# Optimization experiments

Hardware: AMD Instinct MI355X
Metric: run time of the kernel (lower is better)

## Reference

```python
import jax, jax.numpy as jnp
import numpy as np

B, S, D_IN, D_H = 64, 512, 512, 1024

def setup_inputs() -> dict:
    key = jax.random.key(0)
    k1, k2 = jax.random.split(key)
    x = jax.random.normal(k1, (B, S, D_IN), dtype=jnp.float32)
    h0 = jnp.zeros((B, D_H), dtype=jnp.float32)
    # torch Linear(in+hid -> hid): weight [hid, in+hid]; we store transposed [in+hid, hid]
    W = jax.random.normal(k2, (D_IN + D_H, D_H), dtype=jnp.float32) * (1.0 / np.sqrt(D_IN + D_H))
    b = jnp.zeros((D_H,), dtype=jnp.float32)
    return {"x": x, "h0": h0, "W": W, "b": b}

def reference(x, h0, W, b):
    # h_t = tanh([x_t, h_{t-1}] @ W + b). Split W so the input projection
    # is one big batched GEMM outside the scan; recurrence handles Wh part.
    d_in = x.shape[-1]
    Wx, Wh = W[:d_in], W[d_in:]              # [D_in, H], [H, H]
    xproj = jnp.einsum('bsd,dh->bsh', x, Wx) + b  # [B, S, H]

    def step(h, xp_t):
        h_new = jnp.tanh(xp_t + h @ Wh)      # [B, H]
        return h_new, h_new

    # scan over time: move seq axis to front
    h_last, outs = jax.lax.scan(step, h0, jnp.swapaxes(xproj, 0, 1))
    return jnp.swapaxes(outs, 0, 1), h_last  # [B, S, H], [B, H]
```

## Files before the change

### kernel.cpp

```cpp
#include <hip/hip_runtime.h>
#include <hip/hip_bf16.h>
#include <stdint.h>

#define B_   64
#define S_   512
#define DIN  512
#define DH   1024
#define KTOT (DIN + DH)
#define NBG  4
#define NCG  32
#define BBLK 16
#define CBLK 32
#define NKC  (KTOT / 32)
#define NKX  (DIN / 32)

typedef __bf16 bf16x8 __attribute__((ext_vector_type(8)));
typedef float f32x4 __attribute__((ext_vector_type(4)));
typedef unsigned short ushort8v __attribute__((ext_vector_type(8)));
typedef unsigned short ushort4v __attribute__((ext_vector_type(4)));

static __device__ __forceinline__ unsigned short f2bf(float f) {
    union { __bf16 b; unsigned short u; } v; v.b = (__bf16)f; return v.u;
}
static __device__ __forceinline__ float fast_tanh(float x) {
    float e = __expf(2.0f * x);
    return 1.0f - 2.0f / (e + 1.0f);
}

__global__ void k_cvt_bf16(const float* __restrict__ src,
                           unsigned short* __restrict__ dst, int n4) {
    int i = blockIdx.x * blockDim.x + threadIdx.x;
    if (i < n4) {
        float4 v = ((const float4*)src)[i];
        ushort4v o;
        o.x = f2bf(v.x); o.y = f2bf(v.y); o.z = f2bf(v.z); o.w = f2bf(v.w);
        ((ushort4v*)dst)[i] = o;
    }
}

__global__ void k_swz_w(const float* __restrict__ W,
                        unsigned short* __restrict__ dst) {
    int u = blockIdx.x * blockDim.x + threadIdx.x;
    int lane = u & 63;
    int ntg  = (u >> 6) & 63;
    int kc   = u >> 12;
    int q = lane >> 4, n16 = lane & 15;
    int k0 = kc * 32 + q * 8;
    int n  = ntg * 16 + n16;
    ushort8v o;
#pragma unroll
    for (int i = 0; i < 8; ++i) o[i] = f2bf(W[(size_t)(k0 + i) * DH + n]);
    *(ushort8v*)(dst + (size_t)u * 8) = o;
}

#define SMEM_W_USH   (NKC * 2 * 64 * 8)
#define SMEM_P_PITCH 34
#define SMEM_P_FLT   (4 * 16 * SMEM_P_PITCH)
#define SMEM_BYTES   (SMEM_W_USH * 2 + SMEM_P_FLT * 4)

__global__ __launch_bounds__(256, 1) void k_rnn(
    const unsigned short* __restrict__ xb,
    const unsigned short* __restrict__ wswz,
    const float* __restrict__ h0,
    const float* __restrict__ bias,
    float* __restrict__ out,
    unsigned int* ring,
    int* flags)
{
    extern __shared__ char smem[];
    unsigned short* ldsW = (unsigned short*)smem;
    float* ldsP = (float*)(smem + SMEM_W_USH * 2);

    const int tid = threadIdx.x;
    const int bg = blockIdx.x >> 5;
    const int cg = blockIdx.x & 31;
    const int b0 = bg * BBLK;
    const int c0 = cg * CBLK;
    const int lane = tid & 63;
    const int wv = tid >> 6;
    const int q = lane >> 4;
    const int m16 = lane & 15;

    for (int c = tid; c < NKC * 2 * 64; c += 256) {
        int kc = c >> 7;
        int rem = c & 127;
        int l = rem >> 6;
        int ln = rem & 63;
        size_t src = ((size_t)(kc * 64 + 2 * cg + l) * 64 + ln) * 8;
        int dst = ((kc * 2 + l) * 64 + ln) * 8;
        *(ushort8v*)(ldsW + dst) = *(const ushort8v*)(wswz + src);
    }

    const int em = tid >> 4;
    const int np = (tid & 15) * 2;
    const float bias0 = bias[c0 + np];
    const float bias1 = bias[c0 + np + 1];

    __syncthreads();

    for (int t = 0; t < S_; ++t) {
        f32x4 acc0 = {0.f, 0.f, 0.f, 0.f}, acc1 = {0.f, 0.f, 0.f, 0.f};
        {
            bf16x8 ax[4];
            const unsigned short* xrow =
                xb + ((size_t)(b0 + m16) * S_ + t) * DIN + q * 8;
#pragma unroll
            for (int kk = 0; kk < 4; ++kk)
                ax[kk] = *(const bf16x8*)(xrow + (wv * 4 + kk) * 32);
#pragma unroll
            for (int kk = 0; kk < 4; ++kk) {
                int kc = wv * 4 + kk;
                bf16x8 bb0 = *(const bf16x8*)(ldsW + ((kc * 2 + 0) * 64 + lane) * 8);
                bf16x8 bb1 = *(const bf16x8*)(ldsW + ((kc * 2 + 1) * 64 + lane) * 8);
                acc0 = __builtin_amdgcn_mfma_f32_16x16x32_bf16(ax[kk], bb0, acc0, 0, 0, 0);
                acc1 = __builtin_amdgcn_mfma_f32_16x16x32_bf16(ax[kk], bb1, acc1, 0, 0, 0);
            }
        }

        if (t > 0) {
            if (wv == 0) {
                const int* fb = flags + ((size_t)bg * S_ + (t - 1)) * 32;
                for (;;) {
                    int f = __hip_atomic_load(fb + (lane & 31), __ATOMIC_RELAXED,
                                              __HIP_MEMORY_SCOPE_AGENT);
                    if (__all(f != 0)) break;
                    __builtin_amdgcn_s_sleep(1);
                }
            }
            __syncthreads();
        }

        bf16x8 ah[8];
        if (t == 0) {
            const float* hrow = h0 + (size_t)(b0 + m16) * DH + q * 8;
#pragma unroll
            for (int kk = 0; kk < 8; ++kk) {
                const float* p = hrow + (wv * 8 + kk) * 32;
                float4 lo = *(const float4*)(p);
                float4 hi = *(const float4*)(p + 4);
                union { ushort8v s; bf16x8 v; } cv;
                cv.s[0] = f2bf(lo.x); cv.s[1] = f2bf(lo.y);
                cv.s[2] = f2bf(lo.z); cv.s[3] = f2bf(lo.w);
                cv.s[4] = f2bf(hi.x); cv.s[5] = f2bf(hi.y);
                cv.s[6] = f2bf(hi.z); cv.s[7] = f2bf(hi.w);
                ah[kk] = cv.v;
            }
        } else {
            const unsigned long long* rg =
                (const unsigned long long*)(ring + ((t - 1) & 1) * (B_ * (DH / 2)));
            const size_t base = (size_t)(b0 + m16) * 256 + wv * 64 + q * 2;
            unsigned long long w0[8], w1[8];
#pragma unroll
            for (int kk = 0; kk < 8; ++kk) {
                w0[kk] = __hip_atomic_load(rg + base + kk * 8, __ATOMIC_RELAXED,
                                           __HIP_MEMORY_SCOPE_AGENT);
                w1[kk] = __hip_atomic_load(rg + base + kk * 8 + 1, __ATOMIC_RELAXED,
                                           __HIP_MEMORY_SCOPE_AGENT);
            }
#pragma unroll
            for (int kk = 0; kk < 8; ++kk) {
                union { unsigned long long u[2]; bf16x8 v; } cv;
                cv.u[0] = w0[kk]; cv.u[1] = w1[kk];
                ah[kk] = cv.v;
            }
        }

#pragma unroll
        for (int kk = 0; kk < 8; ++kk) {
            int kc = NKX + wv * 8 + kk;
            bf16x8 bb0 = *(const bf16x8*)(ldsW + ((kc * 2 + 0) * 64 + lane) * 8);
            bf16x8 bb1 = *(const bf16x8*)(ldsW + ((kc * 2 + 1) * 64 + lane) * 8);
            acc0 = __builtin_amdgcn_mfma_f32_16x16x32_bf16(ah[kk], bb0, acc0, 0, 0, 0);
            acc1 = __builtin_amdgcn_mfma_f32_16x16x32_bf16(ah[kk], bb1, acc1, 0, 0, 0);
        }
#pragma unroll
        for (int i = 0; i < 4; ++i) {
            ldsP[wv * (16 * SMEM_P_PITCH) + (q * 4 + i) * SMEM_P_PITCH + m16]      = acc0[i];
            ldsP[wv * (16 * SMEM_P_PITCH) + (q * 4 + i) * SMEM_P_PITCH + 16 + m16] = acc1[i];
        }
        __syncthreads();

        float s0 = bias0, s1 = bias1;
#pragma unroll
        for (int w = 0; w < 4; ++w) {
            const float2 p = *(const float2*)(ldsP + w * (16 * SMEM_P_PITCH) +
                                              em * SMEM_P_PITCH + np);
            s0 += p.x; s1 += p.y;
        }
        float v0 = fast_tanh(s0), v1 = fast_tanh(s1);

        unsigned int pk = (unsigned int)f2bf(v0) | ((unsigned int)f2bf(v1) << 16);
        unsigned int* rw = ring + (t & 1) * (B_ * (DH / 2));
        __hip_atomic_store(rw + (size_t)(b0 + em) * (DH / 2) + (c0 + np) / 2, pk,
                           __ATOMIC_RELAXED, __HIP_MEMORY_SCOPE_AGENT);

        __syncthreads();
        if (tid == 0)
            __hip_atomic_store(flags + ((size_t)bg * S_ + t) * 32 + cg, 1,
                               __ATOMIC_RELEASE, __HIP_MEMORY_SCOPE_AGENT);

        float2 ov; ov.x = v0; ov.y = v1;
        *(float2*)(out + ((size_t)(b0 + em) * S_ + t) * DH + c0 + np) = ov;
        if (t == S_ - 1)
            *(float2*)(out + (size_t)B_ * S_ * DH + (size_t)(b0 + em) * DH + c0 + np) = ov;
    }
}

extern "C" void kernel_launch(void* const* d_in, const int* in_sizes, int n_in,
                              void* d_out, int out_size, void* d_ws, size_t ws_size,
                              hipStream_t stream) {
    const float* x  = (const float*)d_in[0];
    const float* h0 = (const float*)d_in[1];
    const float* W  = (const float*)d_in[2];
    const float* b  = (const float*)d_in[3];
    float* out = (float*)d_out;

    char* ws = (char*)d_ws;
    int* flags = (int*)ws;
    unsigned int* ring = (unsigned int*)(ws + 262144);
    unsigned short* xb = (unsigned short*)(ws + 524288);
    unsigned short* wswz = xb + (size_t)B_ * S_ * DIN;

    (void)hipFuncSetAttribute((const void*)k_rnn,
                              hipFuncAttributeMaxDynamicSharedMemorySize,
                              SMEM_BYTES);

    hipMemsetAsync(flags, 0, (size_t)NBG * S_ * 32 * sizeof(int), stream);
    k_cvt_bf16<<<(B_ * S_ * DIN / 4 + 255) / 256, 256, 0, stream>>>(x, xb, B_ * S_ * DIN / 4);
    k_swz_w<<<(NKC * 64 * 64) / 256, 256, 0, stream>>>(W, wswz);
    k_rnn<<<NBG * NCG, 256, SMEM_BYTES, stream>>>(xb, wswz, h0, b, out, ring, flags);
}
```

Before: 3.142 ms.

## Replace per-step flag barrier with sentinel-tagged 4-slot hidden-state ring

Removes the separate per-timestep flag array and the wave-0 spin plus block barrier that waited for all 32 column groups. Each wave now polls the hidden-state values it needs directly, treating 0xFFFFFFFF as not-ready, and producers reset the slot two steps back to the sentinel in a 4-slot ring. This cuts a release store, a flag poll round trip and a __syncthreads from the critical serial path, and lets the first h loads be issued before the x-projection MFMAs. The cost is wider polling traffic and reliance on no valid bf16 pair matching the sentinel (NaN pattern), plus relaxed-ordering correctness of per-word visibility.

```diff
diff --git a/kernel.cpp b/kernel.cpp
--- a/kernel.cpp
+++ b/kernel.cpp
@@ -14,6 +14,10 @@
 #define NKC  (KTOT / 32)
 #define NKX  (DIN / 32)
 
+#define RING_SLOT (B_ * (DH / 2))
+#define NSLOT 4
+#define SENT  0xFFFFFFFFu
+
 typedef __bf16 bf16x8 __attribute__((ext_vector_type(8)));
 typedef float f32x4 __attribute__((ext_vector_type(4)));
 typedef unsigned short ushort8v __attribute__((ext_vector_type(8)));
@@ -64,8 +68,7 @@
     const float* __restrict__ h0,
     const float* __restrict__ bias,
     float* __restrict__ out,
-    unsigned int* ring,
-    int* flags)
+    unsigned int* ring)
 {
     extern __shared__ char smem[];
     unsigned short* ldsW = (unsigned short*)smem;
@@ -96,9 +99,24 @@
     const float bias0 = bias[c0 + np];
     const float bias1 = bias[c0 + np + 1];
 
+    const size_t hbase = (size_t)(b0 + m16) * 256 + (size_t)wv * 64 + (size_t)q * 2;
+
     __syncthreads();
 
     for (int t = 0; t < S_; ++t) {
+        const unsigned long long* rg = (const unsigned long long*)
+            (ring + (size_t)((t - 1) & 3) * RING_SLOT);
+        unsigned long long w[16];
+        if (t > 0) {
+#pragma unroll
+            for (int kk = 0; kk < 8; ++kk) {
+                w[2 * kk]     = __hip_atomic_load(rg + hbase + kk * 8,
+                                  __ATOMIC_RELAXED, __HIP_MEMORY_SCOPE_AGENT);
+                w[2 * kk + 1] = __hip_atomic_load(rg + hbase + kk * 8 + 1,
+                                  __ATOMIC_RELAXED, __HIP_MEMORY_SCOPE_AGENT);
+            }
+        }
+
         f32x4 acc0 = {0.f, 0.f, 0.f, 0.f}, acc1 = {0.f, 0.f, 0.f, 0.f};
         {
             bf16x8 ax[4];
@@ -115,19 +133,6 @@
                 acc0 = __builtin_amdgcn_mfma_f32_16x16x32_bf16(ax[kk], bb0, acc0, 0, 0, 0);
                 acc1 = __builtin_amdgcn_mfma_f32_16x16x32_bf16(ax[kk], bb1, acc1, 0, 0, 0);
             }
-        }
-
-        if (t > 0) {
-            if (wv == 0) {
-                const int* fb = flags + ((size_t)bg * S_ + (t - 1)) * 32;
-                for (;;) {
-                    int f = __hip_atomic_load(fb + (lane & 31), __ATOMIC_RELAXED,
-                                              __HIP_MEMORY_SCOPE_AGENT);
-                    if (__all(f != 0)) break;
-                    __builtin_amdgcn_s_sleep(1);
-                }
-            }
-            __syncthreads();
         }
 
         bf16x8 ah[8];
@@ -146,21 +151,26 @@
                 ah[kk] = cv.v;
             }
         } else {
-            const unsigned long long* rg =
-                (const unsigned long long*)(ring + ((t - 1) & 1) * (B_ * (DH / 2)));
-            const size_t base = (size_t)(b0 + m16) * 256 + wv * 64 + q * 2;
-            unsigned long long w0[8], w1[8];
-#pragma unroll
-            for (int kk = 0; kk < 8; ++kk) {
-                w0[kk] = __hip_atomic_load(rg + base + kk * 8, __ATOMIC_RELAXED,
-                                           __HIP_MEMORY_SCOPE_AGENT);
-                w1[kk] = __hip_atomic_load(rg + base + kk * 8 + 1, __ATOMIC_RELAXED,
-                                           __HIP_MEMORY_SCOPE_AGENT);
+            for (;;) {
+                int ok = 1;
+#pragma unroll
+                for (int j = 0; j < 16; ++j)
+                    ok &= ((unsigned)(w[j] & 0xFFFFFFFFull) != SENT) &
+                          ((unsigned)(w[j] >> 32) != SENT);
+                if (__all(ok)) break;
+                __builtin_amdgcn_s_sleep(1);
+#pragma unroll
+                for (int kk = 0; kk < 8; ++kk) {
+                    w[2 * kk]     = __hip_atomic_load(rg + hbase + kk * 8,
+                                      __ATOMIC_RELAXED, __HIP_MEMORY_SCOPE_AGENT);
+                    w[2 * kk + 1] = __hip_atomic_load(rg + hbase + kk * 8 + 1,
+                                      __ATOMIC_RELAXED, __HIP_MEMORY_SCOPE_AGENT);
+                }
             }
 #pragma unroll
             for (int kk = 0; kk < 8; ++kk) {
                 union { unsigned long long u[2]; bf16x8 v; } cv;
-                cv.u[0] = w0[kk]; cv.u[1] = w1[kk];
+                cv.u[0] = w[2 * kk]; cv.u[1] = w[2 * kk + 1];
                 ah[kk] = cv.v;
             }
         }
@@ -182,22 +192,23 @@
 
         float s0 = bias0, s1 = bias1;
 #pragma unroll
-        for (int w = 0; w < 4; ++w) {
-            const float2 p = *(const float2*)(ldsP + w * (16 * SMEM_P_PITCH) +
+        for (int wq = 0; wq < 4; ++wq) {
+            const float2 p = *(const float2*)(ldsP + wq * (16 * SMEM_P_PITCH) +
                                               em * SMEM_P_PITCH + np);
             s0 += p.x; s1 += p.y;
         }
+        __syncthreads();
+
         float v0 = fast_tanh(s0), v1 = fast_tanh(s1);
 
         unsigned int pk = (unsigned int)f2bf(v0) | ((unsigned int)f2bf(v1) << 16);
-        unsigned int* rw = ring + (t & 1) * (B_ * (DH / 2));
-        __hip_atomic_store(rw + (size_t)(b0 + em) * (DH / 2) + (c0 + np) / 2, pk,
+        const size_t widx = (size_t)(b0 + em) * (DH / 2) + (size_t)(c0 + np) / 2;
+        __hip_atomic_store(ring + (size_t)(t & 3) * RING_SLOT + widx, pk,
                            __ATOMIC_RELAXED, __HIP_MEMORY_SCOPE_AGENT);
 
-        __syncthreads();
-        if (tid == 0)
-            __hip_atomic_store(flags + ((size_t)bg * S_ + t) * 32 + cg, 1,
-                               __ATOMIC_RELEASE, __HIP_MEMORY_SCOPE_AGENT);
+        if (t >= 2)
+            __hip_atomic_store(ring + (size_t)((t - 2) & 3) * RING_SLOT + widx, SENT,
+                               __ATOMIC_RELAXED, __HIP_MEMORY_SCOPE_AGENT);
 
         float2 ov; ov.x = v0; ov.y = v1;
         *(float2*)(out + ((size_t)(b0 + em) * S_ + t) * DH + c0 + np) = ov;
@@ -216,17 +227,16 @@
     float* out = (float*)d_out;
 
     char* ws = (char*)d_ws;
-    int* flags = (int*)ws;
-    unsigned int* ring = (unsigned int*)(ws + 262144);
-    unsigned short* xb = (unsigned short*)(ws + 524288);
+    unsigned int* ring = (unsigned int*)ws;
+    unsigned short* xb = (unsigned short*)(ws + (size_t)NSLOT * RING_SLOT * 4);
     unsigned short* wswz = xb + (size_t)B_ * S_ * DIN;
 
     (void)hipFuncSetAttribute((const void*)k_rnn,
                               hipFuncAttributeMaxDynamicSharedMemorySize,
                               SMEM_BYTES);
 
-    hipMemsetAsync(flags, 0, (size_t)NBG * S_ * 32 * sizeof(int), stream);
+    hipMemsetAsync(ring, 0xFF, (size_t)NSLOT * RING_SLOT * 4, stream);
     k_cvt_bf16<<<(B_ * S_ * DIN / 4 + 255) / 256, 256, 0, stream>>>(x, xb, B_ * S_ * DIN / 4);
     k_swz_w<<<(NKC * 64 * 64) / 256, 256, 0, stream>>>(W, wswz);
-    k_rnn<<<NBG * NCG, 256, SMEM_BYTES, stream>>>(xb, wswz, h0, b, out, ring, flags);
-}
+    k_rnn<<<NBG * NCG, 256, SMEM_BYTES, stream>>>(xb, wswz, h0, b, out, ring);
+}
```

Result: faster. 2.733 ms (-13.0%).
